# Optimization experiments

Measured on AMD Instinct MI355X. Metric: run time of the kernel, lower is better.

The kernel has to match this reference:

```python
import jax, jax.numpy as jnp
import numpy as np

N_NODES = 20000
N_EDGES = 640000
N_TRIP = 1000000
C = 128          # channels
E = 64           # expansion_features
CUTOFF = 5.0
LOG2 = float(np.log(2.0))


def ssp(x):
    # ShiftedSoftplus
    return jax.nn.softplus(x) - LOG2


def setup_inputs() -> dict:
    key = jax.random.key(0)
    ks = jax.random.split(key, 12)
    features = jax.random.normal(ks[0], (N_NODES, C), dtype=jnp.float32)
    neighbour_distances = jax.random.uniform(ks[1], (N_EDGES,), dtype=jnp.float32) * (1.2 * CUTOFF)
    neighbour_list = jax.random.randint(ks[2], (2, N_EDGES), 0, N_NODES, dtype=jnp.int32)
    triplet_idxs = jax.random.randint(ks[3], (N_TRIP, 3), 0, N_NODES, dtype=jnp.int32)
    angles = jax.random.uniform(ks[4], (N_TRIP,), dtype=jnp.float32) * np.pi
    r_ij = jax.random.uniform(ks[5], (N_TRIP,), dtype=jnp.float32) * CUTOFF
    r_ik = jax.random.uniform(ks[6], (N_TRIP,), dtype=jnp.float32) * CUTOFF
    # learned parameters (Linear layers without bias; stored [in, out])
    W_pre = jax.random.normal(ks[7], (C, C), dtype=jnp.float32) / np.sqrt(C)
    W2b1 = jax.random.normal(ks[8], (E, E), dtype=jnp.float32) / np.sqrt(E)
    W2b2 = jax.random.normal(ks[9], (E, C), dtype=jnp.float32) / np.sqrt(E)
    W3b1 = jax.random.normal(ks[10], (3, C // 2), dtype=jnp.float32) / np.sqrt(3.0)
    W3b2 = jax.random.normal(ks[11], (C // 2, C), dtype=jnp.float32) / np.sqrt(C // 2)
    W_post = jax.random.normal(jax.random.fold_in(key, 99), (C, C), dtype=jnp.float32) / np.sqrt(C)
    return {
        "features": features,
        "neighbour_distances": neighbour_distances,
        "neighbour_list": neighbour_list,
        "triplet_idxs": triplet_idxs,
        "angles": angles,
        "r_ij": r_ij,
        "r_ik": r_ik,
        "W_pre": W_pre,
        "W2b1": W2b1,
        "W2b2": W2b2,
        "W3b1": W3b1,
        "W3b2": W3b2,
        "W_post": W_post,
    }


def reference(features, neighbour_distances, neighbour_list, triplet_idxs,
              angles, r_ij, r_ik, W_pre, W2b1, W2b2, W3b1, W3b2, W_post):
    # 1) pre-linear
    h = features @ W_pre                                   # [N, C]

    # 2) radial basis (Gaussian smearing) with smooth cosine cutoff envelope
    centers = jnp.linspace(0.0, CUTOFF, E, dtype=jnp.float32)  # [E]
    width = CUTOFF / E
    gamma = 1.0 / (2.0 * width * width)
    d = neighbour_distances[:, None]                       # [n_edges, 1]
    rb = jnp.exp(-gamma * (d - centers) ** 2)              # [n_edges, E]
    cutoff_mask = (neighbour_distances < CUTOFF).astype(jnp.float32)
    cutoff_values = 0.5 * (1.0 + jnp.cos(np.pi * neighbour_distances / CUTOFF))
    rb = rb * (cutoff_values * cutoff_mask)[:, None]       # fused envelope

    # 3) two-body messages: gather neighbour node features, modulate by radial MLP
    neighbor_h = h[neighbour_list[1]]                      # [n_edges, C]
    two_body = neighbor_h * (ssp(rb @ W2b1) @ W2b2)        # [n_edges, C]

    # 4) three-body messages: angular MLP on (r_ij, r_ik, cos(angle)),
    #    gather node features at triplet_idxs[:,1], scatter-add into edge slots
    tbf = jnp.stack([r_ij, r_ik, jnp.cos(angles)], axis=-1)  # [n_trip, 3]
    w3 = ssp(tbf @ W3b1) @ W3b2                              # [n_trip, C]
    msgs = h[triplet_idxs[:, 1]] * w3                        # [n_trip, C]
    edge_msgs = jnp.zeros_like(two_body).at[triplet_idxs[:, 1]].add(msgs)

    # 5) aggregate messages over neighbours (to central atom = neighbour_list[0])
    messages = two_body + edge_msgs
    agg = jax.ops.segment_sum(messages, neighbour_list[0], num_segments=N_NODES)

    # 6) post-linear
    return agg @ W_post
```

## Files before the change

kernel.cpp:

```cpp
#include <hip/hip_runtime.h>
#include <hip/hip_fp16.h>
#include <math.h>

#define TID threadIdx.x

typedef ushort u16x8 __attribute__((ext_vector_type(8)));
typedef unsigned char uchar;

static constexpr int NN = 20000;
static constexpr int NE = 640000;
static constexpr int NT = 1000000;
static constexpr int C = 128;
static constexpr int E = 64;
static constexpr int LUTN = 4104;
static constexpr int NBKT = 313;
static constexpr int NB2 = 512;
static constexpr int CHE2 = 1250;
static constexpr int CHT2 = 1954;
static constexpr float CUT = 5.0f;
static constexpr float LN2 = 0.69314718055994530942f;

__device__ __forceinline__ float ssp(float x) {
    return fmaxf(x, 0.0f) + __logf(1.0f + __expf(-fabsf(x))) - LN2;
}

__device__ __forceinline__ ushort f2bf(float x) {
    uint u = __float_as_uint(x);
    return (ushort)((u + 0x7FFFu + ((u >> 16) & 1u)) >> 16);
}

__device__ __forceinline__ float bf2f(ushort u) {
    return __uint_as_float((uint)u << 16);
}

__device__ __forceinline__ float h2f(uint bits) {
    return __half2float(__ushort_as_half((ushort)(bits & 0xFFFFu)));
}

__global__ __launch_bounds__(256) void k_gemm16f(const float* __restrict__ A,
                                                 const float* __restrict__ W,
                                                 float* __restrict__ out, int nrows) {
    __shared__ ushort wB[C * C];
    __shared__ float aL[16][132];
    for (int i = TID; i < C * C / 4; i += 256) {
        float4 w4 = ((const float4*)W)[i];
        ushort4 u = {f2bf(w4.x), f2bf(w4.y), f2bf(w4.z), f2bf(w4.w)};
        ((ushort4*)wB)[i] = u;
    }
    const int base = blockIdx.x * 16;
    for (int i = TID; i < 512; i += 256) {
        int r = base + (i >> 5);
        float4 v = (r < nrows) ? ((const float4*)A)[(size_t)r * 32 + (i & 31)]
                               : (float4){0.f, 0.f, 0.f, 0.f};
        *(float4*)&aL[i >> 5][(i & 31) << 2] = v;
    }
    __syncthreads();
    const int rg = TID >> 4;
    const int c8 = (TID & 15) << 3;
    float acc[8] = {0.f, 0.f, 0.f, 0.f, 0.f, 0.f, 0.f, 0.f};
    #pragma unroll 8
    for (int k = 0; k < C; ++k) {
        float a = aL[rg][k];
        u16x8 wv = *(const u16x8*)&wB[k * C + c8];
        #pragma unroll
        for (int j = 0; j < 8; ++j) acc[j] = fmaf(a, bf2f(wv[j]), acc[j]);
    }
    int r = base + rg;
    if (r < nrows) {
        float4 o0 = {acc[0], acc[1], acc[2], acc[3]};
        float4 o1 = {acc[4], acc[5], acc[6], acc[7]};
        *(float4*)&out[(size_t)r * C + c8] = o0;
        *(float4*)&out[(size_t)r * C + c8 + 4] = o1;
    }
}

__global__ __launch_bounds__(256) void k_gemm16b(const float* __restrict__ A,
                                                 const float* __restrict__ W,
                                                 ushort* __restrict__ outB, int nrows) {
    __shared__ ushort wB[C * C];
    __shared__ float aL[16][132];
    for (int i = TID; i < C * C / 4; i += 256) {
        float4 w4 = ((const float4*)W)[i];
        ushort4 u = {f2bf(w4.x), f2bf(w4.y), f2bf(w4.z), f2bf(w4.w)};
        ((ushort4*)wB)[i] = u;
    }
    const int base = blockIdx.x * 16;
    for (int i = TID; i < 512; i += 256) {
        int r = base + (i >> 5);
        float4 v = (r < nrows) ? ((const float4*)A)[(size_t)r * 32 + (i & 31)]
                               : (float4){0.f, 0.f, 0.f, 0.f};
        *(float4*)&aL[i >> 5][(i & 31) << 2] = v;
    }
    __syncthreads();
    const int rg = TID >> 4;
    const int c8 = (TID & 15) << 3;
    float acc[8] = {0.f, 0.f, 0.f, 0.f, 0.f, 0.f, 0.f, 0.f};
    #pragma unroll 8
    for (int k = 0; k < C; ++k) {
        float a = aL[rg][k];
        u16x8 wv = *(const u16x8*)&wB[k * C + c8];
        #pragma unroll
        for (int j = 0; j < 8; ++j) acc[j] = fmaf(a, bf2f(wv[j]), acc[j]);
    }
    int r = base + rg;
    if (r < nrows) {
        u16x8 u;
        #pragma unroll
        for (int j = 0; j < 8; ++j) u[j] = f2bf(acc[j]);
        *(u16x8*)&outB[(size_t)r * C + c8] = u;
    }
}

__global__ __launch_bounds__(256) void k_lut(const float* __restrict__ W2b1,
                                             const float* __restrict__ W2b2,
                                             ushort* __restrict__ lutB,
                                             float2* __restrict__ spLut) {
    if (blockIdx.x == (LUTN + 7) / 8) {
        for (int e = TID; e < 512; e += 256) {
            float t0 = (float)e * (1.0f / 32.0f);
            float t1 = (float)(e + 1) * (1.0f / 32.0f);
            float v0 = log1pf(__expf(-t0));
            float v1 = log1pf(__expf(-t1));
            spLut[e] = make_float2(v0, v1 - v0);
        }
        return;
    }
    __shared__ float w1[E * E];
    __shared__ float w2[E * C];
    __shared__ float rbL[8][E];
    __shared__ float hid[8][E];
    for (int i = TID; i < E * E; i += 256) w1[i] = W2b1[i];
    for (int i = TID; i < E * C; i += 256) w2[i] = W2b2[i];
    const int jj = TID & 63;
    const int esA = TID >> 6;
    const int eg = TID >> 5;
    const int c4 = (TID & 31) << 2;
    const float gamma = 81.92f;
    const float cstep = CUT / 63.0f;
    const float delta = CUT / 4096.0f;
    const int base = blockIdx.x * 8;
    __syncthreads();
    #pragma unroll
    for (int s = 0; s < 2; ++s) {
        int es = esA + 4 * s;
        float d = (float)(base + es) * delta;
        float cv = (d < CUT) ? 0.5f * (1.0f + __cosf((float)M_PI * d / CUT)) : 0.0f;
        float dd = d - (float)jj * cstep;
        rbL[es][jj] = __expf(-gamma * dd * dd) * cv;
    }
    __syncthreads();
    #pragma unroll
    for (int s = 0; s < 2; ++s) {
        int es = esA + 4 * s;
        float a = 0.f;
        #pragma unroll 16
        for (int k = 0; k < E; ++k)
            a = fmaf(rbL[es][k], w1[k * E + jj], a);
        hid[es][jj] = ssp(a);
    }
    __syncthreads();
    float4 o = {0.f, 0.f, 0.f, 0.f};
    #pragma unroll
    for (int j = 0; j < E; ++j) {
        float t = hid[eg][j];
        const float4 w4 = *(const float4*)&w2[j * C + c4];
        o.x = fmaf(t, w4.x, o.x);
        o.y = fmaf(t, w4.y, o.y);
        o.z = fmaf(t, w4.z, o.z);
        o.w = fmaf(t, w4.w, o.w);
    }
    int row = base + eg;
    if (row < LUTN) {
        ushort4 u = {f2bf(o.x), f2bf(o.y), f2bf(o.z), f2bf(o.w)};
        *(ushort4*)&lutB[(size_t)row * C + c4] = u;
    }
}

__global__ __launch_bounds__(256) void k_bcount(const int* __restrict__ nl0,
                                                const int* __restrict__ tidx,
                                                uchar* __restrict__ cntE,
                                                uchar* __restrict__ cntT) {
    __shared__ int h[NBKT];
    const int b = blockIdx.x;
    for (int i = TID; i < NBKT; i += 256) h[i] = 0;
    __syncthreads();
    const int e0 = b * CHE2, e1 = min(e0 + CHE2, NE);
    for (int i = e0 + TID; i < e1; i += 256) atomicAdd(&h[nl0[i] >> 6], 1);
    __syncthreads();
    for (int i = TID; i < NBKT; i += 256) { cntE[(size_t)i * NB2 + b] = (uchar)h[i]; h[i] = 0; }
    __syncthreads();
    const int t0 = b * CHT2, t1 = min(t0 + CHT2, NT);
    for (int i = t0 + TID; i < t1; i += 256) atomicAdd(&h[tidx[3 * i + 1] >> 6], 1);
    __syncthreads();
    for (int i = TID; i < NBKT; i += 256) cntT[(size_t)i * NB2 + b] = (uchar)h[i];
}

__global__ __launch_bounds__(256) void k_bscan(const uchar* __restrict__ cE,
                                               const uchar* __restrict__ cT,
                                               ushort* __restrict__ baseE,
                                               ushort* __restrict__ baseT,
                                               int* __restrict__ totEb,
                                               int* __restrict__ totTb) {
    const int lane = TID & 63;
    const int wv = TID >> 6;
    int task = blockIdx.x * 4 + wv;
    if (task >= 2 * NBKT) return;
    const bool isE = task < NBKT;
    const int k = isE ? task : task - NBKT;
    const uchar* src = isE ? cE : cT;
    ushort* dst = isE ? baseE : baseT;
    int* dT = isE ? totEb : totTb;
    int v[8], pre[8], s = 0;
    #pragma unroll
    for (int j = 0; j < 8; ++j) {
        v[j] = src[(size_t)k * NB2 + lane * 8 + j];
        pre[j] = s;
        s += v[j];
    }
    int incl = s;
    #pragma unroll
    for (int off = 1; off < 64; off <<= 1) {
        int t = __shfl_up(incl, off, 64);
        if (lane >= off) incl += t;
    }
    int excl = incl - s;
    #pragma unroll
    for (int j = 0; j < 8; ++j)
        dst[(size_t)k * NB2 + lane * 8 + j] = (ushort)(excl + pre[j]);
    if (lane == 63) dT[k] = incl;
}

__device__ void scan_one(const int* __restrict__ hist, int* __restrict__ start, int n) {
    __shared__ int wsum[16];
    __shared__ int carryS;
    const int lane = TID & 63;
    const int wv = TID >> 6;
    if (TID == 0) carryS = 0;
    __syncthreads();
    for (int base = 0; base < n; base += 1024) {
        int i = base + TID;
        int v = (i < n) ? hist[i] : 0;
        int acc = v;
        #pragma unroll
        for (int off = 1; off < 64; off <<= 1) {
            int t = __shfl_up(acc, off, 64);
            if (lane >= off) acc += t;
        }
        if (lane == 63) wsum[wv] = acc;
        __syncthreads();
        int woff = 0;
        for (int w = 0; w < wv; ++w) woff += wsum[w];
        int excl = carryS + woff + acc - v;
        if (i < n) start[i] = excl;
        __syncthreads();
        if (TID == 1023) carryS = excl + v;
        __syncthreads();
    }
}

__global__ __launch_bounds__(1024) void k_bktscan(const int* __restrict__ totEb, int* __restrict__ bksE,
                                                  const int* __restrict__ totTb, int* __restrict__ bksT) {
    if (blockIdx.x == 0) scan_one(totEb, bksE, NBKT);
    else                 scan_one(totTb, bksT, NBKT);
}

__global__ __launch_bounds__(256) void k_bplace(const int* __restrict__ nl0,
                                                const int* __restrict__ nl1,
                                                const float* __restrict__ dist,
                                                const int* __restrict__ tidx,
                                                const float* __restrict__ angles,
                                                const float* __restrict__ rij,
                                                const float* __restrict__ rik,
                                                const ushort* __restrict__ baseE,
                                                const ushort* __restrict__ baseT,
                                                const int* __restrict__ bksE,
                                                const int* __restrict__ bksT,
                                                int2* __restrict__ eT,
                                                int2* __restrict__ tT) {
    __shared__ int cur[NBKT];
    const int b = blockIdx.x;
    for (int k = TID; k < NBKT; k += 256)
        cur[k] = bksE[k] + (int)baseE[(size_t)k * NB2 + b];
    __syncthreads();
    const int e0 = b * CHE2, e1 = min(e0 + CHE2, NE);
    for (int i = e0 + TID; i < e1; i += 256) {
        int n0 = nl0[i];
        int pos = atomicAdd(&cur[n0 >> 6], 1);
        uint tq = (uint)fmaf(dist[i], 209715.2f, 0.5f);
        eT[pos] = make_int2((int)(tq | ((uint)(n0 & 63) << 26)), nl1[i]);
    }
    __syncthreads();
    for (int k = TID; k < NBKT; k += 256)
        cur[k] = bksT[k] + (int)baseT[(size_t)k * NB2 + b];
    __syncthreads();
    const int t0 = b * CHT2, tEnd = min(t0 + CHT2, NT);
    for (int i = t0 + TID; i < tEnd; i += 256) {
        int t1 = tidx[3 * i + 1];
        int pos = atomicAdd(&cur[t1 >> 6], 1);
        uint ab = ((uint)__half_as_ushort(__float2half_rn(rik[i])) << 16)
                | (uint)__half_as_ushort(__float2half_rn(rij[i]));
        uint cc = (uint)__half_as_ushort(__float2half_rn(__cosf(angles[i])))
                | ((uint)(t1 & 63) << 16);
        tT[pos] = make_int2((int)ab, (int)cc);
    }
}

__global__ __launch_bounds__(256) void k_nsort(const int2* __restrict__ eTs,
                                               const int2* __restrict__ tTs,
                                               const int* __restrict__ bksE,
                                               const int* __restrict__ bksT,
                                               const int* __restrict__ totEb,
                                               const int* __restrict__ totTb,
                                               int2* __restrict__ eS,
                                               int2* __restrict__ tS,
                                               int* __restrict__ startE,
                                               int* __restrict__ totE,
                                               int* __restrict__ startT,
                                               int* __restrict__ totT) {
    __shared__ int hist[64];
    __shared__ int cur[64];
    const bool isE = blockIdx.x < NBKT;
    const int bkt = isE ? blockIdx.x : blockIdx.x - NBKT;
    const int2* src = isE ? eTs : tTs;
    int2* dst = isE ? eS : tS;
    const int s0 = isE ? bksE[bkt] : bksT[bkt];
    const int cnt = isE ? totEb[bkt] : totTb[bkt];
    int* stX = isE ? startE : startT;
    int* ttX = isE ? totE : totT;
    if (TID < 64) hist[TID] = 0;
    __syncthreads();
    for (int i = TID; i < cnt; i += 256) {
        int2 p = src[s0 + i];
        int nlo = isE ? (int)(((uint)p.x >> 26) & 63u) : (int)(((uint)p.y >> 16) & 63u);
        atomicAdd(&hist[nlo], 1);
    }
    __syncthreads();
    if (TID < 64) {
        int v = hist[TID];
        int incl = v;
        #pragma unroll
        for (int off = 1; off < 64; off <<= 1) {
            int t = __shfl_up(incl, off, 64);
            if (TID >= off) incl += t;
        }
        int excl = incl - v;
        cur[TID] = s0 + excl;
        int node = bkt * 64 + TID;
        if (node < NN) { stX[node] = s0 + excl; ttX[node] = v; }
    }
    __syncthreads();
    for (int i = TID; i < cnt; i += 256) {
        int2 p = src[s0 + i];
        int nlo = isE ? (int)(((uint)p.x >> 26) & 63u) : (int)(((uint)p.y >> 16) & 63u);
        int pos = atomicAdd(&cur[nlo], 1);
        dst[pos] = p;
    }
}

__global__ __launch_bounds__(256) void k_edges_node(const int2* __restrict__ eS,
                                                    const int* __restrict__ startE,
                                                    const int* __restrict__ totE,
                                                    const ushort* __restrict__ hB,
                                                    const ushort* __restrict__ lutB,
                                                    float* __restrict__ agg) {
    __shared__ int4 stage[4][2][64];
    const int lane = TID & 63;
    const int wv = TID >> 6;
    const int c2b = lane << 2;
    for (int r = blockIdx.x * 4 + wv; r < NN; r += gridDim.x * 4) {
        const int s0 = startE[r];
        const int cnt = totE[r];
        float a0 = 0.f, a1 = 0.f;
        int2 pf;
        if (lane < min(64, cnt)) pf = eS[s0 + lane];
        const int nch = (cnt + 63) >> 6;
        for (int c = 0; c < nch; ++c) {
            const int base = c << 6;
            const int n = min(64, cnt - base);
            const int slot = c & 1;
            if (lane < n) {
                uint tq = ((uint)pf.x) & 0x03FFFFFFu;
                int idx = min((int)(tq >> 8), LUTN - 2);
                float fr = (float)(tq & 255u) * (1.0f / 256.0f);
                stage[wv][slot][lane] = make_int4(idx * (C * 2), __float_as_int(fr),
                                                  pf.y * (C * 2), 0);
            }
            int nb = base + 64;
            if (nb < cnt && lane < cnt - nb) pf = eS[s0 + nb + lane];
            asm volatile("s_waitcnt lgkmcnt(0)" ::: "memory");
            #pragma unroll 8
            for (int i = 0; i < n; ++i) {
                int4 q = stage[wv][slot][i];
                float fr = __int_as_float(q.y);
                ushort2 A2 = *(const ushort2*)((const char*)lutB + q.x + c2b);
                ushort2 B2 = *(const ushort2*)((const char*)lutB + q.x + 256 + c2b);
                ushort2 H2 = *(const ushort2*)((const char*)hB + q.z + c2b);
                float ax = bf2f(A2.x), ay = bf2f(A2.y);
                float ox = fmaf(fr, bf2f(B2.x) - ax, ax);
                float oy = fmaf(fr, bf2f(B2.y) - ay, ay);
                a0 = fmaf(ox, bf2f(H2.x), a0);
                a1 = fmaf(oy, bf2f(H2.y), a1);
            }
        }
        asm volatile("s_waitcnt lgkmcnt(0)" ::: "memory");
        float2 o = {a0, a1};
        *(float2*)&agg[(size_t)r * C + (lane << 1)] = o;
    }
}

__global__ __launch_bounds__(256) void k_trip_node(const int* __restrict__ startT,
                                                   const int* __restrict__ totT,
                                                   const int2* __restrict__ tS,
                                                   const float* __restrict__ W3b1,
                                                   const float2* __restrict__ spLut,
                                                   float* __restrict__ uacc) {
    __shared__ uint spl[512];
    __shared__ float4 stage[4][2][64];
    for (int i = TID; i < 512; i += 256) {
        float2 vs = spLut[i];
        spl[i] = ((uint)f2bf(vs.y) << 16) | (uint)f2bf(vs.x);
    }
    __syncthreads();
    const int lane = TID & 63;
    const int wv = TID >> 6;
    const float w1a = W3b1[lane];
    const float w1b = W3b1[64 + lane];
    const float w1c = W3b1[128 + lane];
    for (int r = blockIdx.x * 4 + wv; r < NN; r += gridDim.x * 4) {
        const int s0 = startT[r];
        const int cnt = totT[r];
        float usA = 0.f, usB = 0.f;
        uint2 pf;
        if (lane < min(64, cnt)) pf = ((const uint2*)tS)[s0 + lane];
        const int nch = (cnt + 63) >> 6;
        for (int c = 0; c < nch; ++c) {
            const int base = c << 6;
            const int n = min(64, cnt - base);
            const int slot = c & 1;
            if (lane < n) {
                float4 f;
                f.x = h2f(pf.x);
                f.y = h2f(pf.x >> 16);
                f.z = h2f(pf.y);
                f.w = 0.f;
                stage[wv][slot][lane] = f;
            }
            int nb = base + 64;
            if (nb < cnt && lane < cnt - nb) pf = ((const uint2*)tS)[s0 + nb + lane];
            asm volatile("s_waitcnt lgkmcnt(0)" ::: "memory");
            int i = 0;
            #pragma unroll 4
            for (; i + 1 < n; i += 2) {
                float4 pa = stage[wv][slot][i];
                float4 pb = stage[wv][slot][i + 1];
                float xa = fmaf(pa.x, w1a, fmaf(pa.y, w1b, pa.z * w1c));
                float xb = fmaf(pb.x, w1a, fmaf(pb.y, w1b, pb.z * w1c));
                float ta = fabsf(xa) * 32.0f;
                float tb = fabsf(xb) * 32.0f;
                int ia = min((int)ta, 511);
                int ib = min((int)tb, 511);
                float fa = ta - (float)ia;
                float fb = tb - (float)ib;
                uint va = spl[ia];
                uint vb = spl[ib];
                usA += fmaxf(xa, 0.f) + fmaf(fa, bf2f((ushort)(va >> 16)), bf2f((ushort)va));
                usB += fmaxf(xb, 0.f) + fmaf(fb, bf2f((ushort)(vb >> 16)), bf2f((ushort)vb));
            }
            if (i < n) {
                float4 pa = stage[wv][slot][i];
                float xa = fmaf(pa.x, w1a, fmaf(pa.y, w1b, pa.z * w1c));
                float ta = fabsf(xa) * 32.0f;
                int ia = min((int)ta, 511);
                float fa = ta - (float)ia;
                uint va = spl[ia];
                usA += fmaxf(xa, 0.f) + fmaf(fa, bf2f((ushort)(va >> 16)), bf2f((ushort)va));
            }
        }
        asm volatile("s_waitcnt lgkmcnt(0)" ::: "memory");
        uacc[(size_t)r * 64 + lane] = usA + usB - LN2 * (float)cnt;
    }
}

__global__ __launch_bounds__(256) void k_node_final(const float* __restrict__ uacc,
                                                    const float* __restrict__ W3b2,
                                                    const ushort* __restrict__ hB,
                                                    const int* __restrict__ nl0,
                                                    float* __restrict__ agg) {
    __shared__ uint w2p[64 * 64];
    __shared__ float uL[16][68];
    for (int i = TID; i < 4096; i += 256) {
        int k = i >> 6, l = i & 63;
        w2p[i] = ((uint)f2bf(W3b2[k * C + 64 + l]) << 16) | (uint)f2bf(W3b2[k * C + l]);
    }
    const int base = blockIdx.x * 16;
    {
        int i = TID;
        int row = i >> 4, col = (i & 15) << 2;
        float4 v = ((const float4*)uacc)[(size_t)(base + row) * 16 + (i & 15)];
        *(float4*)&uL[row][col] = v;
    }
    __syncthreads();
    const int lane = TID & 63;
    const int wv = TID >> 6;
    #pragma unroll
    for (int j = 0; j < 4; ++j) {
        const int row = wv * 4 + j;
        float o0 = 0.f, o1 = 0.f;
        #pragma unroll 8
        for (int k = 0; k < 64; ++k) {
            float a = uL[row][k];
            uint wp = w2p[k * 64 + lane];
            o0 = fmaf(a, __uint_as_float(wp << 16), o0);
            o1 = fmaf(a, __uint_as_float(wp & 0xFFFF0000u), o1);
        }
        const int r = base + row;
        const int n0 = nl0[r];
        float h0 = bf2f(hB[(size_t)r * C + lane]);
        float h1 = bf2f(hB[(size_t)r * C + 64 + lane]);
        unsafeAtomicAdd(&agg[(size_t)n0 * C + lane], o0 * h0);
        unsafeAtomicAdd(&agg[(size_t)n0 * C + 64 + lane], o1 * h1);
    }
}

extern "C" void kernel_launch(void* const* d_in, const int* in_sizes, int n_in,
                              void* d_out, int out_size, void* d_ws, size_t ws_size,
                              hipStream_t stream) {
    const float* features = (const float*)d_in[0];
    const float* ndist    = (const float*)d_in[1];
    const int*   nlist    = (const int*)d_in[2];
    const int*   tidx     = (const int*)d_in[3];
    const float* angles   = (const float*)d_in[4];
    const float* rij      = (const float*)d_in[5];
    const float* rik      = (const float*)d_in[6];
    const float* W_pre    = (const float*)d_in[7];
    const float* W2b1     = (const float*)d_in[8];
    const float* W2b2     = (const float*)d_in[9];
    const float* W3b1     = (const float*)d_in[10];
    const float* W3b2     = (const float*)d_in[11];
    const float* W_post   = (const float*)d_in[12];
    float* out = (float*)d_out;

    char* w = (char*)d_ws;
    float* agg    = (float*)w;
    int2* eT      = (int2*)w;
    w += (size_t)NN * C * 4;
    ushort* hB    = (ushort*)w;  w += (size_t)NN * C * 2;
    ushort* lutB  = (ushort*)w;  w += (size_t)LUTN * C * 2;
    int2* eS      = (int2*)w;    w += (size_t)NE * 8;
    int2* tS      = (int2*)w;    w += (size_t)NT * 8;
    int2* tT      = (int2*)w;
    float* uacc   = (float*)w;
    w += (size_t)NT * 8;
    uchar* cntE   = (uchar*)w;   w += (size_t)NBKT * NB2;
    uchar* cntT   = (uchar*)w;   w += (size_t)NBKT * NB2;
    ushort* baseE = (ushort*)w;  w += (size_t)NBKT * NB2 * 2;
    ushort* baseT = (ushort*)w;  w += (size_t)NBKT * NB2 * 2;
    int* totEb    = (int*)w;     w += 1280;
    int* totTb    = (int*)w;     w += 1280;
    int* bksE     = (int*)w;     w += 1280;
    int* bksT     = (int*)w;     w += 1280;
    int* startE   = (int*)w;     w += (size_t)NN * 4;
    int* totE     = (int*)w;     w += (size_t)NN * 4;
    int* startT   = (int*)w;     w += (size_t)NN * 4;
    int* totT     = (int*)w;     w += (size_t)NN * 4;
    float2* spLut = (float2*)w;  w += 512 * 8;

    const int* nl0 = nlist;
    const int* nl1 = nlist + NE;

    hipLaunchKernelGGL(k_gemm16b, dim3((NN + 15) / 16), dim3(256), 0, stream,
                       features, W_pre, hB, NN);
    hipLaunchKernelGGL(k_lut, dim3((LUTN + 7) / 8 + 1), dim3(256), 0, stream,
                       W2b1, W2b2, lutB, spLut);
    hipLaunchKernelGGL(k_bcount, dim3(NB2), dim3(256), 0, stream,
                       nl0, tidx, cntE, cntT);
    hipLaunchKernelGGL(k_bscan, dim3((2 * NBKT + 3) / 4), dim3(256), 0, stream,
                       cntE, cntT, baseE, baseT, totEb, totTb);
    hipLaunchKernelGGL(k_bktscan, dim3(2), dim3(1024), 0, stream,
                       totEb, bksE, totTb, bksT);
    hipLaunchKernelGGL(k_bplace, dim3(NB2), dim3(256), 0, stream,
                       nl0, nl1, ndist, tidx, angles, rij, rik,
                       baseE, baseT, bksE, bksT, eT, tT);
    hipLaunchKernelGGL(k_nsort, dim3(2 * NBKT), dim3(256), 0, stream,
                       eT, tT, bksE, bksT, totEb, totTb,
                       eS, tS, startE, totE, startT, totT);
    hipLaunchKernelGGL(k_trip_node, dim3(2048), dim3(256), 0, stream,
                       startT, totT, tS, W3b1, spLut, uacc);
    hipLaunchKernelGGL(k_edges_node, dim3(2048), dim3(256), 0, stream,
                       eS, startE, totE, hB, lutB, agg);
    hipLaunchKernelGGL(k_node_final, dim3(NN / 16), dim3(256), 0, stream,
                       uacc, W3b2, hB, nl0, agg);
    hipLaunchKernelGGL(k_gemm16f, dim3((NN + 15) / 16), dim3(256), 0, stream,
                       agg, W_post, out, NN);
}
```

Before: 190.0 us.

## Merge independent front kernels and edge/triplet consumers into combined launches

The pre-linear GEMM, radial LUT build and bucket counting kernels are merged into one launch that dispatches on block index over a shared-memory union. The edge and triplet per-node consumer kernels are likewise merged into one launch split between 1024 edge blocks and 1024 triplet blocks. This removes launch gaps and lets independent work overlap on the GPU. In exchange, all blocks reserve the largest shared-memory footprint, which can lower occupancy for the lighter roles.

```diff
diff --git a/kernel.cpp b/kernel.cpp
--- a/kernel.cpp
+++ b/kernel.cpp
@@ -17,6 +17,10 @@
 static constexpr int NB2 = 512;
 static constexpr int CHE2 = 1250;
 static constexpr int CHT2 = 1954;
+static constexpr int G_GEMM = (NN + 15) / 16;
+static constexpr int G_LUT = (LUTN + 7) / 8 + 1;
+static constexpr int G_CONS_E = 1024;
+static constexpr int G_CONS_T = 1024;
 static constexpr float CUT = 5.0f;
 static constexpr float LN2 = 0.69314718055994530942f;
 
@@ -37,162 +41,132 @@
     return __half2float(__ushort_as_half((ushort)(bits & 0xFFFFu)));
 }
 
-__global__ __launch_bounds__(256) void k_gemm16f(const float* __restrict__ A,
-                                                 const float* __restrict__ W,
-                                                 float* __restrict__ out, int nrows) {
-    __shared__ ushort wB[C * C];
-    __shared__ float aL[16][132];
-    for (int i = TID; i < C * C / 4; i += 256) {
-        float4 w4 = ((const float4*)W)[i];
-        ushort4 u = {f2bf(w4.x), f2bf(w4.y), f2bf(w4.z), f2bf(w4.w)};
-        ((ushort4*)wB)[i] = u;
-    }
-    const int base = blockIdx.x * 16;
-    for (int i = TID; i < 512; i += 256) {
-        int r = base + (i >> 5);
-        float4 v = (r < nrows) ? ((const float4*)A)[(size_t)r * 32 + (i & 31)]
-                               : (float4){0.f, 0.f, 0.f, 0.f};
-        *(float4*)&aL[i >> 5][(i & 31) << 2] = v;
-    }
-    __syncthreads();
-    const int rg = TID >> 4;
-    const int c8 = (TID & 15) << 3;
-    float acc[8] = {0.f, 0.f, 0.f, 0.f, 0.f, 0.f, 0.f, 0.f};
-    #pragma unroll 8
-    for (int k = 0; k < C; ++k) {
-        float a = aL[rg][k];
-        u16x8 wv = *(const u16x8*)&wB[k * C + c8];
+__global__ __launch_bounds__(256) void k_front(const float* __restrict__ features,
+                                               const float* __restrict__ W_pre,
+                                               ushort* __restrict__ hB,
+                                               const float* __restrict__ W2b1,
+                                               const float* __restrict__ W2b2,
+                                               ushort* __restrict__ lutB,
+                                               float2* __restrict__ spLut,
+                                               const int* __restrict__ nl0,
+                                               const int* __restrict__ tidx,
+                                               uchar* __restrict__ cntE,
+                                               uchar* __restrict__ cntT) {
+    __shared__ __align__(16) char smem[53248];
+    const int bid = blockIdx.x;
+    if (bid < G_GEMM) {
+        ushort* wB = (ushort*)smem;
+        float (*aL)[132] = (float(*)[132])(smem + 32768);
+        for (int i = TID; i < C * C / 4; i += 256) {
+            float4 w4 = ((const float4*)W_pre)[i];
+            ushort4 u = {f2bf(w4.x), f2bf(w4.y), f2bf(w4.z), f2bf(w4.w)};
+            ((ushort4*)wB)[i] = u;
+        }
+        const int base = bid * 16;
+        for (int i = TID; i < 512; i += 256) {
+            int r = base + (i >> 5);
+            float4 v = (r < NN) ? ((const float4*)features)[(size_t)r * 32 + (i & 31)]
+                                : (float4){0.f, 0.f, 0.f, 0.f};
+            *(float4*)&aL[i >> 5][(i & 31) << 2] = v;
+        }
+        __syncthreads();
+        const int rg = TID >> 4;
+        const int c8 = (TID & 15) << 3;
+        float acc[8] = {0.f, 0.f, 0.f, 0.f, 0.f, 0.f, 0.f, 0.f};
+        #pragma unroll 8
+        for (int k = 0; k < C; ++k) {
+            float a = aL[rg][k];
+            u16x8 wv = *(const u16x8*)&wB[k * C + c8];
+            #pragma unroll
+            for (int j = 0; j < 8; ++j) acc[j] = fmaf(a, bf2f(wv[j]), acc[j]);
+        }
+        int r = base + rg;
+        if (r < NN) {
+            u16x8 u;
+            #pragma unroll
+            for (int j = 0; j < 8; ++j) u[j] = f2bf(acc[j]);
+            *(u16x8*)&hB[(size_t)r * C + c8] = u;
+        }
+        return;
+    }
+    if (bid < G_GEMM + G_LUT) {
+        const int lb = bid - G_GEMM;
+        if (lb == G_LUT - 1) {
+            for (int e = TID; e < 512; e += 256) {
+                float t0 = (float)e * (1.0f / 32.0f);
+                float t1 = (float)(e + 1) * (1.0f / 32.0f);
+                float v0 = log1pf(__expf(-t0));
+                float v1 = log1pf(__expf(-t1));
+                spLut[e] = make_float2(v0, v1 - v0);
+            }
+            return;
+        }
+        float* w1 = (float*)smem;
+        float* w2 = (float*)(smem + 16384);
+        float (*rbL)[E] = (float(*)[E])(smem + 49152);
+        float (*hid)[E] = (float(*)[E])(smem + 51200);
+        for (int i = TID; i < E * E; i += 256) w1[i] = W2b1[i];
+        for (int i = TID; i < E * C; i += 256) w2[i] = W2b2[i];
+        const int jj = TID & 63;
+        const int esA = TID >> 6;
+        const int eg = TID >> 5;
+        const int c4 = (TID & 31) << 2;
+        const float gamma = 81.92f;
+        const float cstep = CUT / 63.0f;
+        const float delta = CUT / 4096.0f;
+        const int base = lb * 8;
+        __syncthreads();
         #pragma unroll
-        for (int j = 0; j < 8; ++j) acc[j] = fmaf(a, bf2f(wv[j]), acc[j]);
-    }
-    int r = base + rg;
-    if (r < nrows) {
-        float4 o0 = {acc[0], acc[1], acc[2], acc[3]};
-        float4 o1 = {acc[4], acc[5], acc[6], acc[7]};
-        *(float4*)&out[(size_t)r * C + c8] = o0;
-        *(float4*)&out[(size_t)r * C + c8 + 4] = o1;
-    }
-}
-
-__global__ __launch_bounds__(256) void k_gemm16b(const float* __restrict__ A,
-                                                 const float* __restrict__ W,
-                                                 ushort* __restrict__ outB, int nrows) {
-    __shared__ ushort wB[C * C];
-    __shared__ float aL[16][132];
-    for (int i = TID; i < C * C / 4; i += 256) {
-        float4 w4 = ((const float4*)W)[i];
-        ushort4 u = {f2bf(w4.x), f2bf(w4.y), f2bf(w4.z), f2bf(w4.w)};
-        ((ushort4*)wB)[i] = u;
-    }
-    const int base = blockIdx.x * 16;
-    for (int i = TID; i < 512; i += 256) {
-        int r = base + (i >> 5);
-        float4 v = (r < nrows) ? ((const float4*)A)[(size_t)r * 32 + (i & 31)]
-                               : (float4){0.f, 0.f, 0.f, 0.f};
-        *(float4*)&aL[i >> 5][(i & 31) << 2] = v;
-    }
-    __syncthreads();
-    const int rg = TID >> 4;
-    const int c8 = (TID & 15) << 3;
-    float acc[8] = {0.f, 0.f, 0.f, 0.f, 0.f, 0.f, 0.f, 0.f};
-    #pragma unroll 8
-    for (int k = 0; k < C; ++k) {
-        float a = aL[rg][k];
-        u16x8 wv = *(const u16x8*)&wB[k * C + c8];
+        for (int s = 0; s < 2; ++s) {
+            int es = esA + 4 * s;
+            float d = (float)(base + es) * delta;
+            float cv = (d < CUT) ? 0.5f * (1.0f + __cosf((float)M_PI * d / CUT)) : 0.0f;
+            float dd = d - (float)jj * cstep;
+            rbL[es][jj] = __expf(-gamma * dd * dd) * cv;
+        }
+        __syncthreads();
         #pragma unroll
-        for (int j = 0; j < 8; ++j) acc[j] = fmaf(a, bf2f(wv[j]), acc[j]);
-    }
-    int r = base + rg;
-    if (r < nrows) {
-        u16x8 u;
+        for (int s = 0; s < 2; ++s) {
+            int es = esA + 4 * s;
+            float a = 0.f;
+            #pragma unroll 16
+            for (int k = 0; k < E; ++k)
+                a = fmaf(rbL[es][k], w1[k * E + jj], a);
+            hid[es][jj] = ssp(a);
+        }
+        __syncthreads();
+        float4 o = {0.f, 0.f, 0.f, 0.f};
         #pragma unroll
-        for (int j = 0; j < 8; ++j) u[j] = f2bf(acc[j]);
-        *(u16x8*)&outB[(size_t)r * C + c8] = u;
-    }
-}
-
-__global__ __launch_bounds__(256) void k_lut(const float* __restrict__ W2b1,
-                                             const float* __restrict__ W2b2,
-                                             ushort* __restrict__ lutB,
-                                             float2* __restrict__ spLut) {
-    if (blockIdx.x == (LUTN + 7) / 8) {
-        for (int e = TID; e < 512; e += 256) {
-            float t0 = (float)e * (1.0f / 32.0f);
-            float t1 = (float)(e + 1) * (1.0f / 32.0f);
-            float v0 = log1pf(__expf(-t0));
-            float v1 = log1pf(__expf(-t1));
-            spLut[e] = make_float2(v0, v1 - v0);
+        for (int j = 0; j < E; ++j) {
+            float t = hid[eg][j];
+            const float4 w4 = *(const float4*)&w2[j * C + c4];
+            o.x = fmaf(t, w4.x, o.x);
+            o.y = fmaf(t, w4.y, o.y);
+            o.z = fmaf(t, w4.z, o.z);
+            o.w = fmaf(t, w4.w, o.w);
+        }
+        int row = base + eg;
+        if (row < LUTN) {
+            ushort4 u = {f2bf(o.x), f2bf(o.y), f2bf(o.z), f2bf(o.w)};
+            *(ushort4*)&lutB[(size_t)row * C + c4] = u;
         }
         return;
     }
-    __shared__ float w1[E * E];
-    __shared__ float w2[E * C];
-    __shared__ float rbL[8][E];
-    __shared__ float hid[8][E];
-    for (int i = TID; i < E * E; i += 256) w1[i] = W2b1[i];
-    for (int i = TID; i < E * C; i += 256) w2[i] = W2b2[i];
-    const int jj = TID & 63;
-    const int esA = TID >> 6;
-    const int eg = TID >> 5;
-    const int c4 = (TID & 31) << 2;
-    const float gamma = 81.92f;
-    const float cstep = CUT / 63.0f;
-    const float delta = CUT / 4096.0f;
-    const int base = blockIdx.x * 8;
-    __syncthreads();
-    #pragma unroll
-    for (int s = 0; s < 2; ++s) {
-        int es = esA + 4 * s;
-        float d = (float)(base + es) * delta;
-        float cv = (d < CUT) ? 0.5f * (1.0f + __cosf((float)M_PI * d / CUT)) : 0.0f;
-        float dd = d - (float)jj * cstep;
-        rbL[es][jj] = __expf(-gamma * dd * dd) * cv;
-    }
-    __syncthreads();
-    #pragma unroll
-    for (int s = 0; s < 2; ++s) {
-        int es = esA + 4 * s;
-        float a = 0.f;
-        #pragma unroll 16
-        for (int k = 0; k < E; ++k)
-            a = fmaf(rbL[es][k], w1[k * E + jj], a);
-        hid[es][jj] = ssp(a);
-    }
-    __syncthreads();
-    float4 o = {0.f, 0.f, 0.f, 0.f};
-    #pragma unroll
-    for (int j = 0; j < E; ++j) {
-        float t = hid[eg][j];
-        const float4 w4 = *(const float4*)&w2[j * C + c4];
-        o.x = fmaf(t, w4.x, o.x);
-        o.y = fmaf(t, w4.y, o.y);
-        o.z = fmaf(t, w4.z, o.z);
-        o.w = fmaf(t, w4.w, o.w);
-    }
-    int row = base + eg;
-    if (row < LUTN) {
-        ushort4 u = {f2bf(o.x), f2bf(o.y), f2bf(o.z), f2bf(o.w)};
-        *(ushort4*)&lutB[(size_t)row * C + c4] = u;
-    }
-}
-
-__global__ __launch_bounds__(256) void k_bcount(const int* __restrict__ nl0,
-                                                const int* __restrict__ tidx,
-                                                uchar* __restrict__ cntE,
-                                                uchar* __restrict__ cntT) {
-    __shared__ int h[NBKT];
-    const int b = blockIdx.x;
-    for (int i = TID; i < NBKT; i += 256) h[i] = 0;
-    __syncthreads();
-    const int e0 = b * CHE2, e1 = min(e0 + CHE2, NE);
-    for (int i = e0 + TID; i < e1; i += 256) atomicAdd(&h[nl0[i] >> 6], 1);
-    __syncthreads();
-    for (int i = TID; i < NBKT; i += 256) { cntE[(size_t)i * NB2 + b] = (uchar)h[i]; h[i] = 0; }
-    __syncthreads();
-    const int t0 = b * CHT2, t1 = min(t0 + CHT2, NT);
-    for (int i = t0 + TID; i < t1; i += 256) atomicAdd(&h[tidx[3 * i + 1] >> 6], 1);
-    __syncthreads();
-    for (int i = TID; i < NBKT; i += 256) cntT[(size_t)i * NB2 + b] = (uchar)h[i];
+    {
+        int* h = (int*)smem;
+        const int b = bid - G_GEMM - G_LUT;
+        for (int i = TID; i < NBKT; i += 256) h[i] = 0;
+        __syncthreads();
+        const int e0 = b * CHE2, e1 = min(e0 + CHE2, NE);
+        for (int i = e0 + TID; i < e1; i += 256) atomicAdd(&h[nl0[i] >> 6], 1);
+        __syncthreads();
+        for (int i = TID; i < NBKT; i += 256) { cntE[(size_t)i * NB2 + b] = (uchar)h[i]; h[i] = 0; }
+        __syncthreads();
+        const int t0 = b * CHT2, t1 = min(t0 + CHT2, NT);
+        for (int i = t0 + TID; i < t1; i += 256) atomicAdd(&h[tidx[3 * i + 1] >> 6], 1);
+        __syncthreads();
+        for (int i = TID; i < NBKT; i += 256) cntT[(size_t)i * NB2 + b] = (uchar)h[i];
+    }
 }
 
 __global__ __launch_bounds__(256) void k_bscan(const uchar* __restrict__ cE,
@@ -357,127 +331,130 @@
     }
 }
 
-__global__ __launch_bounds__(256) void k_edges_node(const int2* __restrict__ eS,
-                                                    const int* __restrict__ startE,
-                                                    const int* __restrict__ totE,
-                                                    const ushort* __restrict__ hB,
-                                                    const ushort* __restrict__ lutB,
-                                                    float* __restrict__ agg) {
-    __shared__ int4 stage[4][2][64];
+__global__ __launch_bounds__(256) void k_consume(const int2* __restrict__ eS,
+                                                 const int* __restrict__ startE,
+                                                 const int* __restrict__ totE,
+                                                 const ushort* __restrict__ hB,
+                                                 const ushort* __restrict__ lutB,
+                                                 float* __restrict__ agg,
+                                                 const int2* __restrict__ tS,
+                                                 const int* __restrict__ startT,
+                                                 const int* __restrict__ totT,
+                                                 const float* __restrict__ W3b1,
+                                                 const float2* __restrict__ spLut,
+                                                 float* __restrict__ uacc) {
+    __shared__ __align__(16) char smem[10752];
     const int lane = TID & 63;
     const int wv = TID >> 6;
-    const int c2b = lane << 2;
-    for (int r = blockIdx.x * 4 + wv; r < NN; r += gridDim.x * 4) {
-        const int s0 = startE[r];
-        const int cnt = totE[r];
-        float a0 = 0.f, a1 = 0.f;
-        int2 pf;
-        if (lane < min(64, cnt)) pf = eS[s0 + lane];
-        const int nch = (cnt + 63) >> 6;
-        for (int c = 0; c < nch; ++c) {
-            const int base = c << 6;
-            const int n = min(64, cnt - base);
-            const int slot = c & 1;
-            if (lane < n) {
-                uint tq = ((uint)pf.x) & 0x03FFFFFFu;
-                int idx = min((int)(tq >> 8), LUTN - 2);
-                float fr = (float)(tq & 255u) * (1.0f / 256.0f);
-                stage[wv][slot][lane] = make_int4(idx * (C * 2), __float_as_int(fr),
-                                                  pf.y * (C * 2), 0);
+    if (blockIdx.x < G_CONS_E) {
+        int4 (*stage)[2][64] = (int4(*)[2][64])smem;
+        const int c2b = lane << 2;
+        for (int r = blockIdx.x * 4 + wv; r < NN; r += G_CONS_E * 4) {
+            const int s0 = startE[r];
+            const int cnt = totE[r];
+            float a0 = 0.f, a1 = 0.f;
+            int2 pf;
+            if (lane < min(64, cnt)) pf = eS[s0 + lane];
+            const int nch = (cnt + 63) >> 6;
+            for (int c = 0; c < nch; ++c) {
+                const int base = c << 6;
+                const int n = min(64, cnt - base);
+                const int slot = c & 1;
+                if (lane < n) {
+                    uint tq = ((uint)pf.x) & 0x03FFFFFFu;
+                    int idx = min((int)(tq >> 8), LUTN - 2);
+                    float fr = (float)(tq & 255u) * (1.0f / 256.0f);
+                    stage[wv][slot][lane] = make_int4(idx * (C * 2), __float_as_int(fr),
+                                                      pf.y * (C * 2), 0);
+                }
+                int nb = base + 64;
+                if (nb < cnt && lane < cnt - nb) pf = eS[s0 + nb + lane];
+                asm volatile("s_waitcnt lgkmcnt(0)" ::: "memory");
+                #pragma unroll 8
+                for (int i = 0; i < n; ++i) {
+                    int4 q = stage[wv][slot][i];
+                    float fr = __int_as_float(q.y);
+                    ushort2 A2 = *(const ushort2*)((const char*)lutB + q.x + c2b);
+                    ushort2 B2 = *(const ushort2*)((const char*)lutB + q.x + 256 + c2b);
+                    ushort2 H2 = *(const ushort2*)((const char*)hB + q.z + c2b);
+                    float ax = bf2f(A2.x), ay = bf2f(A2.y);
+                    float ox = fmaf(fr, bf2f(B2.x) - ax, ax);
+                    float oy = fmaf(fr, bf2f(B2.y) - ay, ay);
+                    a0 = fmaf(ox, bf2f(H2.x), a0);
+                    a1 = fmaf(oy, bf2f(H2.y), a1);
+                }
             }
-            int nb = base + 64;
-            if (nb < cnt && lane < cnt - nb) pf = eS[s0 + nb + lane];
             asm volatile("s_waitcnt lgkmcnt(0)" ::: "memory");
-            #pragma unroll 8
-            for (int i = 0; i < n; ++i) {
-                int4 q = stage[wv][slot][i];
-                float fr = __int_as_float(q.y);
-                ushort2 A2 = *(const ushort2*)((const char*)lutB + q.x + c2b);
-                ushort2 B2 = *(const ushort2*)((const char*)lutB + q.x + 256 + c2b);
-                ushort2 H2 = *(const ushort2*)((const char*)hB + q.z + c2b);
-                float ax = bf2f(A2.x), ay = bf2f(A2.y);
-                float ox = fmaf(fr, bf2f(B2.x) - ax, ax);
-                float oy = fmaf(fr, bf2f(B2.y) - ay, ay);
-                a0 = fmaf(ox, bf2f(H2.x), a0);
-                a1 = fmaf(oy, bf2f(H2.y), a1);
+            float2 o = {a0, a1};
+            *(float2*)&agg[(size_t)r * C + (lane << 1)] = o;
+        }
+        return;
+    }
+    {
+        uint* spl = (uint*)smem;
+        float4 (*stage)[2][64] = (float4(*)[2][64])(smem + 2048);
+        for (int i = TID; i < 512; i += 256) {
+            float2 vs = spLut[i];
+            spl[i] = ((uint)f2bf(vs.y) << 16) | (uint)f2bf(vs.x);
+        }
+        __syncthreads();
+        const float w1a = W3b1[lane];
+        const float w1b = W3b1[64 + lane];
+        const float w1c = W3b1[128 + lane];
+        const int bid = blockIdx.x - G_CONS_E;
+        for (int r = bid * 4 + wv; r < NN; r += G_CONS_T * 4) {
+            const int s0 = startT[r];
+            const int cnt = totT[r];
+            float usA = 0.f, usB = 0.f;
+            uint2 pf;
+            if (lane < min(64, cnt)) pf = ((const uint2*)tS)[s0 + lane];
+            const int nch = (cnt + 63) >> 6;
+            for (int c = 0; c < nch; ++c) {
+                const int base = c << 6;
+                const int n = min(64, cnt - base);
+                const int slot = c & 1;
+                if (lane < n) {
+                    float4 f;
+                    f.x = h2f(pf.x);
+                    f.y = h2f(pf.x >> 16);
+                    f.z = h2f(pf.y);
+                    f.w = 0.f;
+                    stage[wv][slot][lane] = f;
+                }
+                int nb = base + 64;
+                if (nb < cnt && lane < cnt - nb) pf = ((const uint2*)tS)[s0 + nb + lane];
+                asm volatile("s_waitcnt lgkmcnt(0)" ::: "memory");
+                int i = 0;
+                #pragma unroll 4
+                for (; i + 1 < n; i += 2) {
+                    float4 pa = stage[wv][slot][i];
+                    float4 pb = stage[wv][slot][i + 1];
+                    float xa = fmaf(pa.x, w1a, fmaf(pa.y, w1b, pa.z * w1c));
+                    float xb = fmaf(pb.x, w1a, fmaf(pb.y, w1b, pb.z * w1c));
+                    float ta = fabsf(xa) * 32.0f;
+                    float tb = fabsf(xb) * 32.0f;
+                    int ia = min((int)ta, 511);
+                    int ib = min((int)tb, 511);
+                    float fa = ta - (float)ia;
+                    float fb = tb - (float)ib;
+                    uint va = spl[ia];
+                    uint vb = spl[ib];
+                    usA += fmaxf(xa, 0.f) + fmaf(fa, bf2f((ushort)(va >> 16)), bf2f((ushort)va));
+                    usB += fmaxf(xb, 0.f) + fmaf(fb, bf2f((ushort)(vb >> 16)), bf2f((ushort)vb));
+                }
+                if (i < n) {
+                    float4 pa = stage[wv][slot][i];
+                    float xa = fmaf(pa.x, w1a, fmaf(pa.y, w1b, pa.z * w1c));
+                    float ta = fabsf(xa) * 32.0f;
+                    int ia = min((int)ta, 511);
+                    float fa = ta - (float)ia;
+                    uint va = spl[ia];
+                    usA += fmaxf(xa, 0.f) + fmaf(fa, bf2f((ushort)(va >> 16)), bf2f((ushort)va));
+                }
             }
-        }
-        asm volatile("s_waitcnt lgkmcnt(0)" ::: "memory");
-        float2 o = {a0, a1};
-        *(float2*)&agg[(size_t)r * C + (lane << 1)] = o;
-    }
-}
-
-__global__ __launch_bounds__(256) void k_trip_node(const int* __restrict__ startT,
-                                                   const int* __restrict__ totT,
-                                                   const int2* __restrict__ tS,
-                                                   const float* __restrict__ W3b1,
-                                                   const float2* __restrict__ spLut,
-                                                   float* __restrict__ uacc) {
-    __shared__ uint spl[512];
-    __shared__ float4 stage[4][2][64];
-    for (int i = TID; i < 512; i += 256) {
-        float2 vs = spLut[i];
-        spl[i] = ((uint)f2bf(vs.y) << 16) | (uint)f2bf(vs.x);
-    }
-    __syncthreads();
-    const int lane = TID & 63;
-    const int wv = TID >> 6;
-    const float w1a = W3b1[lane];
-    const float w1b = W3b1[64 + lane];
-    const float w1c = W3b1[128 + lane];
-    for (int r = blockIdx.x * 4 + wv; r < NN; r += gridDim.x * 4) {
-        const int s0 = startT[r];
-        const int cnt = totT[r];
-        float usA = 0.f, usB = 0.f;
-        uint2 pf;
-        if (lane < min(64, cnt)) pf = ((const uint2*)tS)[s0 + lane];
-        const int nch = (cnt + 63) >> 6;
-        for (int c = 0; c < nch; ++c) {
-            const int base = c << 6;
-            const int n = min(64, cnt - base);
-            const int slot = c & 1;
-            if (lane < n) {
-                float4 f;
-                f.x = h2f(pf.x);
-                f.y = h2f(pf.x >> 16);
-                f.z = h2f(pf.y);
-                f.w = 0.f;
-                stage[wv][slot][lane] = f;
-            }
-            int nb = base + 64;
-            if (nb < cnt && lane < cnt - nb) pf = ((const uint2*)tS)[s0 + nb + lane];
             asm volatile("s_waitcnt lgkmcnt(0)" ::: "memory");
-            int i = 0;
-            #pragma unroll 4
-            for (; i + 1 < n; i += 2) {
-                float4 pa = stage[wv][slot][i];
-                float4 pb = stage[wv][slot][i + 1];
-                float xa = fmaf(pa.x, w1a, fmaf(pa.y, w1b, pa.z * w1c));
-                float xb = fmaf(pb.x, w1a, fmaf(pb.y, w1b, pb.z * w1c));
-                float ta = fabsf(xa) * 32.0f;
-                float tb = fabsf(xb) * 32.0f;
-                int ia = min((int)ta, 511);
-                int ib = min((int)tb, 511);
-                float fa = ta - (float)ia;
-                float fb = tb - (float)ib;
-                uint va = spl[ia];
-                uint vb = spl[ib];
-                usA += fmaxf(xa, 0.f) + fmaf(fa, bf2f((ushort)(va >> 16)), bf2f((ushort)va));
-                usB += fmaxf(xb, 0.f) + fmaf(fb, bf2f((ushort)(vb >> 16)), bf2f((ushort)vb));
-            }
-            if (i < n) {
-                float4 pa = stage[wv][slot][i];
-                float xa = fmaf(pa.x, w1a, fmaf(pa.y, w1b, pa.z * w1c));
-                float ta = fabsf(xa) * 32.0f;
-                int ia = min((int)ta, 511);
-                float fa = ta - (float)ia;
-                uint va = spl[ia];
-                usA += fmaxf(xa, 0.f) + fmaf(fa, bf2f((ushort)(va >> 16)), bf2f((ushort)va));
-            }
-        }
-        asm volatile("s_waitcnt lgkmcnt(0)" ::: "memory");
-        uacc[(size_t)r * 64 + lane] = usA + usB - LN2 * (float)cnt;
+            uacc[(size_t)r * 64 + lane] = usA + usB - LN2 * (float)cnt;
+        }
     }
 }
 
@@ -519,6 +496,43 @@
         float h1 = bf2f(hB[(size_t)r * C + 64 + lane]);
         unsafeAtomicAdd(&agg[(size_t)n0 * C + lane], o0 * h0);
         unsafeAtomicAdd(&agg[(size_t)n0 * C + 64 + lane], o1 * h1);
+    }
+}
+
+__global__ __launch_bounds__(256) void k_gemm16f(const float* __restrict__ A,
+                                                 const float* __restrict__ W,
+                                                 float* __restrict__ out, int nrows) {
+    __shared__ ushort wB[C * C];
+    __shared__ float aL[16][132];
+    for (int i = TID; i < C * C / 4; i += 256) {
+        float4 w4 = ((const float4*)W)[i];
+        ushort4 u = {f2bf(w4.x), f2bf(w4.y), f2bf(w4.z), f2bf(w4.w)};
+        ((ushort4*)wB)[i] = u;
+    }
+    const int base = blockIdx.x * 16;
+    for (int i = TID; i < 512; i += 256) {
+        int r = base + (i >> 5);
+        float4 v = (r < nrows) ? ((const float4*)A)[(size_t)r * 32 + (i & 31)]
+                               : (float4){0.f, 0.f, 0.f, 0.f};
+        *(float4*)&aL[i >> 5][(i & 31) << 2] = v;
+    }
+    __syncthreads();
+    const int rg = TID >> 4;
+    const int c8 = (TID & 15) << 3;
+    float acc[8] = {0.f, 0.f, 0.f, 0.f, 0.f, 0.f, 0.f, 0.f};
+    #pragma unroll 8
+    for (int k = 0; k < C; ++k) {
+        float a = aL[rg][k];
+        u16x8 wv = *(const u16x8*)&wB[k * C + c8];
+        #pragma unroll
+        for (int j = 0; j < 8; ++j) acc[j] = fmaf(a, bf2f(wv[j]), acc[j]);
+    }
+    int r = base + rg;
+    if (r < nrows) {
+        float4 o0 = {acc[0], acc[1], acc[2], acc[3]};
+        float4 o1 = {acc[4], acc[5], acc[6], acc[7]};
+        *(float4*)&out[(size_t)r * C + c8] = o0;
+        *(float4*)&out[(size_t)r * C + c8 + 4] = o1;
     }
 }
 
@@ -568,11 +582,8 @@
     const int* nl0 = nlist;
     const int* nl1 = nlist + NE;
 
-    hipLaunchKernelGGL(k_gemm16b, dim3((NN + 15) / 16), dim3(256), 0, stream,
-                       features, W_pre, hB, NN);
-    hipLaunchKernelGGL(k_lut, dim3((LUTN + 7) / 8 + 1), dim3(256), 0, stream,
-                       W2b1, W2b2, lutB, spLut);
-    hipLaunchKernelGGL(k_bcount, dim3(NB2), dim3(256), 0, stream,
+    hipLaunchKernelGGL(k_front, dim3(G_GEMM + G_LUT + NB2), dim3(256), 0, stream,
+                       features, W_pre, hB, W2b1, W2b2, lutB, spLut,
                        nl0, tidx, cntE, cntT);
     hipLaunchKernelGGL(k_bscan, dim3((2 * NBKT + 3) / 4), dim3(256), 0, stream,
                        cntE, cntT, baseE, baseT, totEb, totTb);
@@ -584,10 +595,9 @@
     hipLaunchKernelGGL(k_nsort, dim3(2 * NBKT), dim3(256), 0, stream,
                        eT, tT, bksE, bksT, totEb, totTb,
                        eS, tS, startE, totE, startT, totT);
-    hipLaunchKernelGGL(k_trip_node, dim3(2048), dim3(256), 0, stream,
-                       startT, totT, tS, W3b1, spLut, uacc);
-    hipLaunchKernelGGL(k_edges_node, dim3(2048), dim3(256), 0, stream,
-                       eS, startE, totE, hB, lutB, agg);
+    hipLaunchKernelGGL(k_consume, dim3(G_CONS_E + G_CONS_T), dim3(256), 0, stream,
+                       eS, startE, totE, hB, lutB, agg,
+                       tS, startT, totT, W3b1, spLut, uacc);
     hipLaunchKernelGGL(k_node_final, dim3(NN / 16), dim3(256), 0, stream,
                        uacc, W3b2, hB, nl0, agg);
     hipLaunchKernelGGL(k_gemm16f, dim3((NN + 15) / 16), dim3(256), 0, stream,
```

Result: faster. 175.4 us (-7.7%).
